# Optimization experiments

Measured on AMD Instinct MI355X. Metric: run time of the kernel, lower is better.

Reference implementation:

```python
import jax, jax.numpy as jnp
import numpy as np

N, H, MSG, OUT = 512, 128, 128, 64
F1, F2 = 256, 256  # f_dims (also used for g_mlp per source)
GOUT = 128         # hardcoded output_gmlp_dim
O1 = 256           # o_dims


def _p(key, shape, scale):
    return jax.random.normal(key, shape, dtype=jnp.float32) * scale


def setup_inputs() -> dict:
    key = jax.random.key(0)
    ks = jax.random.split(key, 24)
    s = lambda fan_in: 1.0 / np.sqrt(fan_in)
    inp = {
        "x": jax.random.normal(ks[0], (N, H), dtype=jnp.float32),
        "hidden": jax.random.normal(ks[1], (N, H), dtype=jnp.float32),
        "h0": jnp.zeros((1, N, H), dtype=jnp.float32),
        "c0": jnp.zeros((1, N, H), dtype=jnp.float32),
        # f MLP: 2H -> F1 -> F2 -> MSG
        "Wf1": _p(ks[2], (F1, 2 * H), s(2 * H)), "bf1": jnp.zeros((F1,), jnp.float32),
        "Wf2": _p(ks[3], (F2, F1), s(F1)), "bf2": jnp.zeros((F2,), jnp.float32),
        "Wf3": _p(ks[4], (MSG, F2), s(F2)), "bf3": jnp.zeros((MSG,), jnp.float32),
        # g_mlp: H+MSG -> F1 -> F2 -> GOUT
        "Wg1": _p(ks[5], (F1, H + MSG), s(H + MSG)), "bg1": jnp.zeros((F1,), jnp.float32),
        "Wg2": _p(ks[6], (F2, F1), s(F1)), "bg2": jnp.zeros((F2,), jnp.float32),
        "Wg3": _p(ks[7], (GOUT, F2), s(F2)), "bg3": jnp.zeros((GOUT,), jnp.float32),
        # LSTM (1 layer): GOUT -> H, gate order i,f,g,o
        "W_ih": _p(ks[8], (4 * H, GOUT), s(H)), "W_hh": _p(ks[9], (4 * H, H), s(H)),
        "b_ih": jnp.zeros((4 * H,), jnp.float32), "b_hh": jnp.zeros((4 * H,), jnp.float32),
        # o MLP: H -> O1 -> OUT
        "Wo1": _p(ks[10], (O1, H), s(H)), "bo1": jnp.zeros((O1,), jnp.float32),
        "Wo2": _p(ks[11], (OUT, O1), s(O1)), "bo2": jnp.zeros((OUT,), jnp.float32),
    }
    return inp


def reference(x, hidden, h0, c0,
              Wf1, bf1, Wf2, bf2, Wf3, bf3,
              Wg1, bg1, Wg2, bg2, Wg3, bg3,
              W_ih, W_hh, b_ih, b_hh,
              Wo1, bo1, Wo2, bo2):
    # --- pairwise message MLP f(cat(hidden[i], hidden[j])) over all (i,j) ---
    # split first-layer weight to avoid materializing [N,N,2H] concat
    A = hidden @ Wf1[:, :H].T            # [N, F1], contribution of node i
    B = hidden @ Wf1[:, H:].T            # [N, F1], contribution of node j
    h1 = jax.nn.relu(A[:, None, :] + B[None, :, :] + bf1)   # [N, N, F1]
    h2 = jax.nn.relu(h1 @ Wf2.T + bf2)                       # [N, N, F2]
    messages = h2 @ Wf3.T + bf3                              # [N, N, MSG]
    sum_messages = jnp.sum(messages, axis=0)                 # [N, MSG] (sum over i)

    # --- g_mlp on cat(x, sum_messages) ---
    g_in = jnp.concatenate([x, sum_messages], axis=1)        # [N, H+MSG]
    g1 = jax.nn.relu(g_in @ Wg1.T + bg1)
    g2 = jax.nn.relu(g1 @ Wg2.T + bg2)
    input_g = g2 @ Wg3.T + bg3                               # [N, GOUT]

    # --- single-step LSTM (seq_len=1, batch=N), PyTorch gate order i,f,g,o ---
    gates = input_g @ W_ih.T + b_ih + h0[0] @ W_hh.T + b_hh  # [N, 4H]
    i_g, f_g, g_g, o_g = jnp.split(gates, 4, axis=1)
    i_g = jax.nn.sigmoid(i_g); f_g = jax.nn.sigmoid(f_g)
    g_g = jnp.tanh(g_g); o_g = jax.nn.sigmoid(o_g)
    c_new = f_g * c0[0] + i_g * g_g
    hidden_new = o_g * jnp.tanh(c_new)                       # [N, H]

    # --- output MLP o (single_output=False) ---
    o1 = jax.nn.relu(hidden_new @ Wo1.T + bo1)
    out = o1 @ Wo2.T + bo2                                   # [N, OUT]

    return (out, hidden_new, hidden_new[None], c_new[None])
```

## Files before the change

kernel.cpp:

```cpp
#include <hip/hip_runtime.h>
#include <hip/hip_bf16.h>


#define NN   512
#define HH   128
#define F1D  256
#define F2D  256
#define OUTD 64
#define ICHUNK 64

typedef _Float16 half_t;
typedef _Float16 half8 __attribute__((ext_vector_type(8)));
typedef float float4_t __attribute__((ext_vector_type(4)));
typedef float float8_t __attribute__((ext_vector_type(8)));

__device__ __forceinline__ float sigmoidf_(float x) {
    return 1.0f / (1.0f + __expf(-x));
}

#define HL_INV 2.44140625e-4f

#define WS_TAIL_B 1835008
#define WS_WT1_B  3342336
#define T3H 0
#define G1H 65536
#define G2H 196608
#define G3H 327680
#define CATH 393216
#define O1H 655360
#define O2H 720896

__constant__ int p_cum[8]   = {16, 24, 40, 56, 64, 96, 112, 116};
__constant__ int p_K[8]     = {256, 256, 256, 256, 256, 256, 128, 256};
__constant__ int p_hioff[8] = {0, T3H, G1H, G2H, G3H, CATH, O1H, O2H};
__constant__ int p_cnt[8]   = {65536, 32768, 65536, 65536, 32768, 131072, 32768, 16384};

__global__ __launch_bounds__(256)
void k0_prep(const float* __restrict__ Wf1,
             const float* __restrict__ Wf2,
             const float* __restrict__ Wf3,
             const float* __restrict__ Wg1, const float* __restrict__ Wg2,
             const float* __restrict__ Wg3,
             const float* __restrict__ W_ih, const float* __restrict__ W_hh,
             const float* __restrict__ Wo1, const float* __restrict__ Wo2,
             half_t* __restrict__ tail,
             half_t* __restrict__ W2H, half_t* __restrict__ W2L,
             float* __restrict__ WT1) {
    __shared__ float slab[4096];
    __shared__ float tile[64][65];
    const int t = threadIdx.x;
    const int bid = blockIdx.x;

    if (bid < 116) {
        int m = 0;
        while (m < 7 && bid >= p_cum[m]) ++m;
        const int pl = bid - (m ? p_cum[m - 1] : 0);
        const int K = p_K[m];
        const int kshift = (K == 256) ? 8 : 7;
        const int n0 = pl * 16;

        const float* src;
        switch (m) {
            case 0: src = Wf2; break;
            case 1: src = Wf3; break;
            case 2: src = Wg1; break;
            case 3: src = Wg2; break;
            case 4: src = Wg3; break;
            case 6: src = Wo1; break;
            default: src = Wo2; break;
        }
        for (int q = t; q < (16 * K) / 4; q += 256) {
            const int flat = q * 4;
            const int r = flat >> kshift;
            const int k = flat & (K - 1);
            float4_t v;
            if (m == 5) {
                v = (k < 128) ? *(const float4_t*)(W_ih + (n0 + r) * 128 + k)
                              : *(const float4_t*)(W_hh + (n0 + r) * 128 + (k - 128));
            } else {
                v = *(const float4_t*)(src + (size_t)(n0 + r) * K + k);
            }
            *(float4_t*)&slab[flat] = v;
        }
        __syncthreads();

        half_t *hi, *lo;
        if (m == 0) { hi = W2H; lo = W2L; }
        else        { hi = tail + p_hioff[m]; lo = hi + p_cnt[m]; }
        const int base = pl * (K << 4);
        for (int f0 = t * 8; f0 < 16 * K; f0 += 2048) {
            const int ks = f0 >> 9;
            const int g4 = (f0 >> 7) & 3;
            const int l15 = (f0 >> 3) & 15;
            const int k0 = ks * 32 + g4 * 8;
            float8_t v = *(const float8_t*)&slab[l15 * K + k0];
            half8 hv, lv;
#pragma unroll
            for (int e = 0; e < 8; ++e) {
                half_t h = (half_t)v[e];
                hv[e] = h;
                lv[e] = (half_t)((v[e] - (float)h) * 4096.0f);
            }
            *(half8*)(hi + base + f0) = hv;
            *(half8*)(lo + base + f0) = lv;
        }
    } else {
        const int local = bid - 116;
        const int tr = local >> 2, tc = local & 3;
#pragma unroll
        for (int q = 0; q < 16; ++q) {
            const int idx = q * 256 + t;
            const int ly = idx >> 6, lx = idx & 63;
            tile[ly][lx] = Wf1[(tr * 64 + ly) * 256 + tc * 64 + lx];
        }
        __syncthreads();
#pragma unroll
        for (int q = 0; q < 16; ++q) {
            const int idx = q * 256 + t;
            const int ly = idx >> 6, lx = idx & 63;
            WT1[(tc * 64 + ly) * 256 + tr * 64 + lx] = tile[lx][ly];
        }
    }
}

__global__ __launch_bounds__(256)
void k1_proj(const float* __restrict__ hidden,
             const float* __restrict__ WT1,
             const float* __restrict__ bf1,
             float* __restrict__ A32,
             float* __restrict__ B32) {
    __shared__ float hid[4][HH];
    const int t = threadIdx.x;
    const int i0 = blockIdx.x * 4;
    for (int q = t; q < 4 * HH; q += 256)
        hid[q >> 7][q & 127] = hidden[(i0 + (q >> 7)) * HH + (q & 127)];
    __syncthreads();

    float accA[4], accB[4];
    const float b = bf1[t];
#pragma unroll
    for (int r = 0; r < 4; ++r) { accA[r] = b; accB[r] = 0.0f; }

    const float* wcol = WT1 + t;
#pragma unroll 4
    for (int kk = 0; kk < HH; ++kk) {
        const float va = wcol[kk * 256];
        const float vb = wcol[(kk + 128) * 256];
#pragma unroll
        for (int r = 0; r < 4; ++r) {
            const float h = hid[r][kk];
            accA[r] = fmaf(h, va, accA[r]);
            accB[r] = fmaf(h, vb, accB[r]);
        }
    }
#pragma unroll
    for (int r = 0; r < 4; ++r) {
        A32[(i0 + r) * F1D + t] = accA[r];
        B32[(i0 + r) * F1D + t] = accB[r];
    }
}

__global__ __launch_bounds__(512, 2)
void k2_pairwise(const float* __restrict__ A32,
                 const float* __restrict__ B32,
                 const half_t* __restrict__ W2H,
                 const half_t* __restrict__ W2L,
                 const float* __restrict__ bf2,
                 float* __restrict__ S) {
    __shared__ half_t hbuf[2][4][8][512];

    const int tid = threadIdx.x;
    const int lane = tid & 63;
    const int w = tid >> 6;
    const int l15 = lane & 15;
    const int g4 = lane >> 4;
    const int j0 = blockIdx.y * 16;
    const int i0 = blockIdx.x * ICHUNK;
    const int lane8 = lane * 8;

    const half8* WH8 = (const half8*)W2H;
    const half8* WL8 = (const half8*)W2L;
    half8 Wh[2][8], Wl[2][8];
#pragma unroll
    for (int nt = 0; nt < 2; ++nt)
#pragma unroll
        for (int ks = 0; ks < 8; ++ks) {
            const int idx = (w * 2 + nt) * 512 + ks * 64 + lane;
            Wh[nt][ks] = WH8[idx];
            Wl[nt][ks] = WL8[idx];
        }
#pragma unroll
    for (int nt = 0; nt < 2; ++nt)
#pragma unroll
        for (int ks = 0; ks < 8; ++ks) {
            asm volatile("" : "+v"(Wh[nt][ks]));
            asm volatile("" : "+v"(Wl[nt][ks]));
        }

    float4_t Bw0 = *(const float4_t*)(B32 + (size_t)(j0 + l15) * F1D + w * 32 + g4 * 8);
    float4_t Bw1 = *(const float4_t*)(B32 + (size_t)(j0 + l15) * F1D + w * 32 + g4 * 8 + 4);

    float b2v[2];
#pragma unroll
    for (int nt = 0; nt < 2; ++nt) b2v[nt] = bf2[w * 32 + nt * 16 + l15];

    float4_t acc[2];
#pragma unroll
    for (int nt = 0; nt < 2; ++nt)
#pragma unroll
        for (int r = 0; r < 4; ++r) acc[nt][r] = 0.0f;

#pragma unroll
    for (int q = 0; q < 4; ++q) {
        const float* Ap = A32 + (size_t)(i0 + q) * F1D + w * 32 + g4 * 8;
        float4_t a0 = *(const float4_t*)Ap;
        float4_t a1 = *(const float4_t*)(Ap + 4);
        half8 hf;
#pragma unroll
        for (int e = 0; e < 4; ++e) {
            hf[e]     = (half_t)fmaxf(a0[e] + Bw0[e], 0.0f);
            hf[4 + e] = (half_t)fmaxf(a1[e] + Bw1[e], 0.0f);
        }
        *(half8*)&hbuf[0][q][w][lane8] = hf;
    }
    __syncthreads();

    for (int c = 0; c < 16; ++c) {
        const int cur = c & 1;
        const int nxt = cur ^ 1;
        const int ibase = i0 + (c + 1) * 4;

#pragma unroll
        for (int q = 0; q < 4; ++q) {
            float4_t a0, a1;
            if (c < 15) {
                const float* Ap = A32 + (size_t)(ibase + q) * F1D + w * 32 + g4 * 8;
                a0 = *(const float4_t*)Ap;
                a1 = *(const float4_t*)(Ap + 4);
            }

            float4_t C[2], Cl[2];
#pragma unroll
            for (int nt = 0; nt < 2; ++nt)
#pragma unroll
                for (int r = 0; r < 4; ++r) { C[nt][r] = 0.0f; Cl[nt][r] = 0.0f; }
#pragma unroll
            for (int ks = 0; ks < 8; ++ks) {
                half8 hf = *(const half8*)&hbuf[cur][q][ks][lane8];
                C[0]  = __builtin_amdgcn_mfma_f32_16x16x32_f16(hf, Wh[0][ks], C[0], 0, 0, 0);
                C[1]  = __builtin_amdgcn_mfma_f32_16x16x32_f16(hf, Wh[1][ks], C[1], 0, 0, 0);
                Cl[0] = __builtin_amdgcn_mfma_f32_16x16x32_f16(hf, Wl[0][ks], Cl[0], 0, 0, 0);
                Cl[1] = __builtin_amdgcn_mfma_f32_16x16x32_f16(hf, Wl[1][ks], Cl[1], 0, 0, 0);
            }

            if (c < 15) {
                half8 hf;
#pragma unroll
                for (int e = 0; e < 4; ++e) {
                    hf[e]     = (half_t)fmaxf(a0[e] + Bw0[e], 0.0f);
                    hf[4 + e] = (half_t)fmaxf(a1[e] + Bw1[e], 0.0f);
                }
                *(half8*)&hbuf[nxt][q][w][lane8] = hf;
            }

#pragma unroll
            for (int nt = 0; nt < 2; ++nt)
#pragma unroll
                for (int r = 0; r < 4; ++r) {
                    float v = fmaf(Cl[nt][r], HL_INV, C[nt][r]) + b2v[nt];
                    acc[nt][r] += fmaxf(v, 0.0f);
                }
        }
        __syncthreads();
    }

#pragma unroll
    for (int nt = 0; nt < 2; ++nt)
#pragma unroll
        for (int r = 0; r < 4; ++r)
            atomicAdd(&S[(size_t)(j0 + g4 * 4 + r) * F2D + w * 32 + nt * 16 + l15], acc[nt][r]);
}

#define AST 260

template<int NT, int NKS>
__device__ __forceinline__ void frag_gemm(const float* __restrict__ aPtr,
                                          const half_t* __restrict__ WhF,
                                          const half_t* __restrict__ WlF,
                                          const int* pB, int lane8,
                                          float4_t* Chi, float4_t* Clo) {
#pragma unroll
    for (int ks = 0; ks < NKS; ++ks) {
        float4_t a0 = *(const float4_t*)(aPtr + ks * 32);
        float4_t a1 = *(const float4_t*)(aPtr + ks * 32 + 4);
        half8 ah, al;
#pragma unroll
        for (int e = 0; e < 4; ++e) {
            half_t h0 = (half_t)a0[e];
            ah[e] = h0; al[e] = (half_t)((a0[e] - (float)h0) * 4096.0f);
            half_t h1 = (half_t)a1[e];
            ah[4+e] = h1; al[4+e] = (half_t)((a1[e] - (float)h1) * 4096.0f);
        }
#pragma unroll
        for (int nt = 0; nt < NT; ++nt) {
            half8 wh = *(const half8*)(WhF + pB[nt] + ks * 512 + lane8);
            half8 wl = *(const half8*)(WlF + pB[nt] + ks * 512 + lane8);
            Chi[nt] = __builtin_amdgcn_mfma_f32_16x16x32_f16(ah, wh, Chi[nt], 0, 0, 0);
            Clo[nt] = __builtin_amdgcn_mfma_f32_16x16x32_f16(ah, wl, Clo[nt], 0, 0, 0);
            Clo[nt] = __builtin_amdgcn_mfma_f32_16x16x32_f16(al, wh, Clo[nt], 0, 0, 0);
        }
    }
}

__global__ __launch_bounds__(512)
void k4_tail(const float* __restrict__ S,
             const float* __restrict__ x,
             const float* __restrict__ h0,
             const float* __restrict__ c0,
             const half_t* __restrict__ tail,
             const float* __restrict__ bf3,
             const float* __restrict__ bg1, const float* __restrict__ bg2,
             const float* __restrict__ bg3,
             const float* __restrict__ b_ih, const float* __restrict__ b_hh,
             const float* __restrict__ bo1, const float* __restrict__ bo2,
             float* __restrict__ out,
             float* __restrict__ hid_out,
             float* __restrict__ h_out,
             float* __restrict__ c_out) {
    __shared__ float bufA[16 * AST];
    __shared__ float bufB[16 * AST];
    __shared__ float bufC[16 * AST];
    const int tid = threadIdx.x;
    const int lane = tid & 63;
    const int w = tid >> 6;
    const int l15 = lane & 15;
    const int g4 = lane >> 4;
    const int r0 = blockIdx.x * 16;
    const int lane8 = lane * 8;

    for (int q = tid; q < 16 * 256; q += 512)
        bufC[(q >> 8) * AST + (q & 255)] = S[(size_t)(r0 + (q >> 8)) * 256 + (q & 255)];
    for (int q = tid; q < 16 * 128; q += 512)
        bufA[(q >> 7) * AST + (q & 127)] = x[(r0 + (q >> 7)) * 128 + (q & 127)];
    __syncthreads();

    const float* aFrag;
    int pB[4];
    float4_t Chi[4], Clo[4];

    {
        const int n = w * 16 + l15;
        pB[0] = w * 4096;
        Chi[0] = float4_t{0,0,0,0}; Clo[0] = float4_t{0,0,0,0};
        aFrag = bufC + l15 * AST + g4 * 8;
        frag_gemm<1, 8>(aFrag, tail + T3H, tail + T3H + 32768, pB, lane8, Chi, Clo);
        const float b = 512.0f * bf3[n];
#pragma unroll
        for (int r = 0; r < 4; ++r)
            bufA[(g4 * 4 + r) * AST + 128 + n] = Chi[0][r] + Clo[0][r] * HL_INV + b;
    }
    __syncthreads();

    {
        pB[0] = (w * 2) * 4096; pB[1] = (w * 2 + 1) * 4096;
        Chi[0] = float4_t{0,0,0,0}; Clo[0] = float4_t{0,0,0,0};
        Chi[1] = float4_t{0,0,0,0}; Clo[1] = float4_t{0,0,0,0};
        aFrag = bufA + l15 * AST + g4 * 8;
        frag_gemm<2, 8>(aFrag, tail + G1H, tail + G1H + 65536, pB, lane8, Chi, Clo);
#pragma unroll
        for (int nt = 0; nt < 2; ++nt) {
            const int n = w * 32 + nt * 16 + l15;
            const float b = bg1[n];
#pragma unroll
            for (int r = 0; r < 4; ++r)
                bufB[(g4 * 4 + r) * AST + n] = fmaxf(Chi[nt][r] + Clo[nt][r] * HL_INV + b, 0.0f);
        }
    }
    __syncthreads();

    {
        pB[0] = (w * 2) * 4096; pB[1] = (w * 2 + 1) * 4096;
        Chi[0] = float4_t{0,0,0,0}; Clo[0] = float4_t{0,0,0,0};
        Chi[1] = float4_t{0,0,0,0}; Clo[1] = float4_t{0,0,0,0};
        aFrag = bufB + l15 * AST + g4 * 8;
        frag_gemm<2, 8>(aFrag, tail + G2H, tail + G2H + 65536, pB, lane8, Chi, Clo);
#pragma unroll
        for (int nt = 0; nt < 2; ++nt) {
            const int n = w * 32 + nt * 16 + l15;
            const float b = bg2[n];
#pragma unroll
            for (int r = 0; r < 4; ++r)
                bufC[(g4 * 4 + r) * AST + n] = fmaxf(Chi[nt][r] + Clo[nt][r] * HL_INV + b, 0.0f);
        }
        for (int q = tid; q < 16 * 128; q += 512)
            bufA[(q >> 7) * AST + 128 + (q & 127)] = h0[(r0 + (q >> 7)) * 128 + (q & 127)];
    }
    __syncthreads();

    {
        const int n = w * 16 + l15;
        pB[0] = w * 4096;
        Chi[0] = float4_t{0,0,0,0}; Clo[0] = float4_t{0,0,0,0};
        aFrag = bufC + l15 * AST + g4 * 8;
        frag_gemm<1, 8>(aFrag, tail + G3H, tail + G3H + 32768, pB, lane8, Chi, Clo);
        const float b = bg3[n];
#pragma unroll
        for (int r = 0; r < 4; ++r)
            bufA[(g4 * 4 + r) * AST + n] = Chi[0][r] + Clo[0][r] * HL_INV + b;
    }
    __syncthreads();

    {
#pragma unroll
        for (int nt = 0; nt < 4; ++nt) {
            pB[nt] = (w + nt * 8) * 4096;
            Chi[nt] = float4_t{0,0,0,0}; Clo[nt] = float4_t{0,0,0,0};
        }
        aFrag = bufA + l15 * AST + g4 * 8;
        frag_gemm<4, 8>(aFrag, tail + CATH, tail + CATH + 131072, pB, lane8, Chi, Clo);

        const int nh = w * 16 + l15;
        float bi = b_ih[nh]       + b_hh[nh];
        float bf = b_ih[128 + nh] + b_hh[128 + nh];
        float bg = b_ih[256 + nh] + b_hh[256 + nh];
        float bo = b_ih[384 + nh] + b_hh[384 + nh];
#pragma unroll
        for (int r = 0; r < 4; ++r) {
            const int row = r0 + g4 * 4 + r;
            float gi = sigmoidf_(Chi[0][r] + Clo[0][r] * HL_INV + bi);
            float gf = sigmoidf_(Chi[1][r] + Clo[1][r] * HL_INV + bf);
            float gg = tanhf(    Chi[2][r] + Clo[2][r] * HL_INV + bg);
            float go = sigmoidf_(Chi[3][r] + Clo[3][r] * HL_INV + bo);
            float c = gf * c0[row * 128 + nh] + gi * gg;
            float h = go * tanhf(c);
            bufC[(g4 * 4 + r) * AST + nh] = h;
            hid_out[row * 128 + nh] = h;
            h_out[row * 128 + nh]   = h;
            c_out[row * 128 + nh]   = c;
        }
    }
    __syncthreads();

    {
        pB[0] = (w * 2) * 2048; pB[1] = (w * 2 + 1) * 2048;
        Chi[0] = float4_t{0,0,0,0}; Clo[0] = float4_t{0,0,0,0};
        Chi[1] = float4_t{0,0,0,0}; Clo[1] = float4_t{0,0,0,0};
        aFrag = bufC + l15 * AST + g4 * 8;
        frag_gemm<2, 4>(aFrag, tail + O1H, tail + O1H + 32768, pB, lane8, Chi, Clo);
#pragma unroll
        for (int nt = 0; nt < 2; ++nt) {
            const int n = w * 32 + nt * 16 + l15;
            const float b = bo1[n];
#pragma unroll
            for (int r = 0; r < 4; ++r)
                bufB[(g4 * 4 + r) * AST + n] = fmaxf(Chi[nt][r] + Clo[nt][r] * HL_INV + b, 0.0f);
        }
    }
    __syncthreads();

    if (w < 4) {
        const int n = w * 16 + l15;
        pB[0] = w * 4096;
        Chi[0] = float4_t{0,0,0,0}; Clo[0] = float4_t{0,0,0,0};
        aFrag = bufB + l15 * AST + g4 * 8;
        frag_gemm<1, 8>(aFrag, tail + O2H, tail + O2H + 16384, pB, lane8, Chi, Clo);
        const float b = bo2[n];
#pragma unroll
        for (int r = 0; r < 4; ++r)
            out[(r0 + g4 * 4 + r) * OUTD + n] = Chi[0][r] + Clo[0][r] * HL_INV + b;
    }
}

extern "C" void kernel_launch(void* const* d_in, const int* in_sizes, int n_in,
                              void* d_out, int out_size, void* d_ws, size_t ws_size,
                              hipStream_t stream) {
    const float* x      = (const float*)d_in[0];
    const float* hidden = (const float*)d_in[1];
    const float* h0     = (const float*)d_in[2];
    const float* c0     = (const float*)d_in[3];
    const float* Wf1    = (const float*)d_in[4];
    const float* bf1    = (const float*)d_in[5];
    const float* Wf2    = (const float*)d_in[6];
    const float* bf2    = (const float*)d_in[7];
    const float* Wf3    = (const float*)d_in[8];
    const float* bf3    = (const float*)d_in[9];
    const float* Wg1    = (const float*)d_in[10];
    const float* bg1    = (const float*)d_in[11];
    const float* Wg2    = (const float*)d_in[12];
    const float* bg2    = (const float*)d_in[13];
    const float* Wg3    = (const float*)d_in[14];
    const float* bg3    = (const float*)d_in[15];
    const float* W_ih   = (const float*)d_in[16];
    const float* W_hh   = (const float*)d_in[17];
    const float* b_ih   = (const float*)d_in[18];
    const float* b_hh   = (const float*)d_in[19];
    const float* Wo1    = (const float*)d_in[20];
    const float* bo1    = (const float*)d_in[21];
    const float* Wo2    = (const float*)d_in[22];
    const float* bo2    = (const float*)d_in[23];

    char* wsb = (char*)d_ws;
    float*  A32  = (float*)(wsb + 0);
    float*  B32  = (float*)(wsb + 524288);
    half_t* W2H  = (half_t*)(wsb + 1048576);
    half_t* W2L  = (half_t*)(wsb + 1179648);
    float*  S    = (float*)(wsb + 1310720);
    half_t* tail = (half_t*)(wsb + WS_TAIL_B);
    float*  WT1  = (float*)(wsb + WS_WT1_B);

    float* outp  = (float*)d_out;
    float* hid1  = (float*)d_out + 32768;
    float* hid2  = (float*)d_out + 98304;
    float* cout  = (float*)d_out + 163840;

    hipMemsetAsync(S, 0, (size_t)NN * F2D * sizeof(float), stream);

    k0_prep<<<dim3(132), dim3(256), 0, stream>>>(Wf1, Wf2, Wf3, Wg1, Wg2, Wg3,
                                                 W_ih, W_hh, Wo1, Wo2,
                                                 tail, W2H, W2L, WT1);

    k1_proj<<<dim3(128), dim3(256), 0, stream>>>(hidden, WT1, bf1, A32, B32);

    k2_pairwise<<<dim3(8, 32), dim3(512), 0, stream>>>(A32, B32, W2H, W2L, bf2, S);

    k4_tail<<<dim3(32), dim3(512), 0, stream>>>(S, x, h0, c0, tail,
                                                bf3, bg1, bg2, bg3,
                                                b_ih, b_hh, bo1, bo2,
                                                outp, hid1, hid2, cout);
}
```

Before: 205.3 us.

## Fuse weight prep, first-layer projection and S zeroing into one kernel

Folds the memset of S, the Wf1 transpose and the k1 projection kernel into the prep kernel. The projection now reads Wf1 rows directly with vector loads instead of going through a transposed copy, so WT1 is no longer needed. This removes two launches and one dependency barrier. In exchange, each thread reads a strided row, so the global loads are less coalesced.

```diff
diff --git a/kernel.cpp b/kernel.cpp
--- a/kernel.cpp
+++ b/kernel.cpp
@@ -21,7 +21,6 @@
 #define HL_INV 2.44140625e-4f
 
 #define WS_TAIL_B 1835008
-#define WS_WT1_B  3342336
 #define T3H 0
 #define G1H 65536
 #define G2H 196608
@@ -36,7 +35,9 @@
 __constant__ int p_cnt[8]   = {65536, 32768, 65536, 65536, 32768, 131072, 32768, 16384};
 
 __global__ __launch_bounds__(256)
-void k0_prep(const float* __restrict__ Wf1,
+void kP_prep(const float* __restrict__ hidden,
+             const float* __restrict__ Wf1,
+             const float* __restrict__ bf1,
              const float* __restrict__ Wf2,
              const float* __restrict__ Wf3,
              const float* __restrict__ Wg1, const float* __restrict__ Wg2,
@@ -45,9 +46,9 @@
              const float* __restrict__ Wo1, const float* __restrict__ Wo2,
              half_t* __restrict__ tail,
              half_t* __restrict__ W2H, half_t* __restrict__ W2L,
-             float* __restrict__ WT1) {
+             float* __restrict__ A32, float* __restrict__ B32,
+             float* __restrict__ S) {
     __shared__ float slab[4096];
-    __shared__ float tile[64][65];
     const int t = threadIdx.x;
     const int bid = blockIdx.x;
 
@@ -105,58 +106,41 @@
             *(half8*)(lo + base + f0) = lv;
         }
     } else {
-        const int local = bid - 116;
-        const int tr = local >> 2, tc = local & 3;
-#pragma unroll
-        for (int q = 0; q < 16; ++q) {
-            const int idx = q * 256 + t;
-            const int ly = idx >> 6, lx = idx & 63;
-            tile[ly][lx] = Wf1[(tr * 64 + ly) * 256 + tc * 64 + lx];
-        }
+        const int pb = bid - 116;
+        const int i0 = pb * 4;
+
+        {
+            float4_t z = {0.0f, 0.0f, 0.0f, 0.0f};
+            *(float4_t*)(S + (size_t)pb * 1024 + t * 4) = z;
+        }
+
+        float* hid = slab;
+        for (int q = t; q < 4 * HH; q += 256)
+            hid[q] = hidden[i0 * HH + q];
         __syncthreads();
-#pragma unroll
-        for (int q = 0; q < 16; ++q) {
-            const int idx = q * 256 + t;
-            const int ly = idx >> 6, lx = idx & 63;
-            WT1[(tc * 64 + ly) * 256 + tr * 64 + lx] = tile[lx][ly];
-        }
-    }
-}
-
-__global__ __launch_bounds__(256)
-void k1_proj(const float* __restrict__ hidden,
-             const float* __restrict__ WT1,
-             const float* __restrict__ bf1,
-             float* __restrict__ A32,
-             float* __restrict__ B32) {
-    __shared__ float hid[4][HH];
-    const int t = threadIdx.x;
-    const int i0 = blockIdx.x * 4;
-    for (int q = t; q < 4 * HH; q += 256)
-        hid[q >> 7][q & 127] = hidden[(i0 + (q >> 7)) * HH + (q & 127)];
-    __syncthreads();
-
-    float accA[4], accB[4];
-    const float b = bf1[t];
-#pragma unroll
-    for (int r = 0; r < 4; ++r) { accA[r] = b; accB[r] = 0.0f; }
-
-    const float* wcol = WT1 + t;
+
+        float accA[4], accB[4];
+        const float b = bf1[t];
+#pragma unroll
+        for (int r = 0; r < 4; ++r) { accA[r] = b; accB[r] = 0.0f; }
+
+        const float* wr = Wf1 + t * 256;
 #pragma unroll 4
-    for (int kk = 0; kk < HH; ++kk) {
-        const float va = wcol[kk * 256];
-        const float vb = wcol[(kk + 128) * 256];
+        for (int k = 0; k < HH; k += 4) {
+            float4_t wa = *(const float4_t*)(wr + k);
+            float4_t wb = *(const float4_t*)(wr + HH + k);
+#pragma unroll
+            for (int r = 0; r < 4; ++r) {
+                const float* hp = &hid[r * HH + k];
+                accA[r] += wa[0]*hp[0] + wa[1]*hp[1] + wa[2]*hp[2] + wa[3]*hp[3];
+                accB[r] += wb[0]*hp[0] + wb[1]*hp[1] + wb[2]*hp[2] + wb[3]*hp[3];
+            }
+        }
 #pragma unroll
         for (int r = 0; r < 4; ++r) {
-            const float h = hid[r][kk];
-            accA[r] = fmaf(h, va, accA[r]);
-            accB[r] = fmaf(h, vb, accB[r]);
-        }
-    }
-#pragma unroll
-    for (int r = 0; r < 4; ++r) {
-        A32[(i0 + r) * F1D + t] = accA[r];
-        B32[(i0 + r) * F1D + t] = accB[r];
+            A32[(i0 + r) * F1D + t] = accA[r];
+            B32[(i0 + r) * F1D + t] = accB[r];
+        }
     }
 }
 
@@ -506,20 +490,17 @@
     half_t* W2L  = (half_t*)(wsb + 1179648);
     float*  S    = (float*)(wsb + 1310720);
     half_t* tail = (half_t*)(wsb + WS_TAIL_B);
-    float*  WT1  = (float*)(wsb + WS_WT1_B);
 
     float* outp  = (float*)d_out;
     float* hid1  = (float*)d_out + 32768;
     float* hid2  = (float*)d_out + 98304;
     float* cout  = (float*)d_out + 163840;
 
-    hipMemsetAsync(S, 0, (size_t)NN * F2D * sizeof(float), stream);
-
-    k0_prep<<<dim3(132), dim3(256), 0, stream>>>(Wf1, Wf2, Wf3, Wg1, Wg2, Wg3,
+    kP_prep<<<dim3(244), dim3(256), 0, stream>>>(hidden, Wf1, bf1, Wf2,
+                                                 Wf3, Wg1, Wg2, Wg3,
                                                  W_ih, W_hh, Wo1, Wo2,
-                                                 tail, W2H, W2L, WT1);
-
-    k1_proj<<<dim3(128), dim3(256), 0, stream>>>(hidden, WT1, bf1, A32, B32);
+                                                 tail, W2H, W2L,
+                                                 A32, B32, S);
 
     k2_pairwise<<<dim3(8, 32), dim3(512), 0, stream>>>(A32, B32, W2H, W2L, bf2, S);
 
```

New measurement: 197.3 us. 1.04x faster.
